# Kernel optimization log

Hardware: AMD Instinct MI355X
Metric: run time of the kernel (lower is better)

Reference implementation:

```python
import jax, jax.numpy as jnp
import numpy as np

B, N, D = 16, 8192, 256
H = D // 2
N_PARCELS = 64          # number of parcel labels in the stage lookup
K_PER_PARCEL = 32       # allocation m for every parcel (self.values)
TAU = 1.0               # gumbel-softmax temperature


def setup_inputs() -> dict:
    key = jax.random.key(0)
    ks = jax.random.split(key, 6)
    patches = jax.random.normal(ks[0], (B, N, D), dtype=jnp.float32)
    features = jax.random.normal(ks[1], (B, N, D), dtype=jnp.float32)
    W1 = jax.random.normal(ks[2], (D, H), dtype=jnp.float32) * 0.05
    b1 = jnp.zeros((H,), dtype=jnp.float32)
    W2 = jax.random.normal(ks[3], (H,), dtype=jnp.float32) * 0.05  # fc2 weight, out_dim=1 squeezed
    b2 = jnp.zeros((), dtype=jnp.float32)
    # pre-sampled Gumbel(0,1) noise (torch F.gumbel_softmax samples internally)
    gumbel = jax.random.gumbel(ks[4], (B, N), dtype=jnp.float32)
    # flat per-patch parcel label, identical across batch (lookup.reshape(-1)[:N])
    lookup = (jnp.arange(N, dtype=jnp.int32) % N_PARCELS)
    return {"patches": patches, "features": features, "W1": W1, "b1": b1,
            "W2": W2, "b2": b2, "gumbel": gumbel, "lookup": lookup}


def reference(patches, features, W1, b1, W2, b2, gumbel, lookup):
    # tiny MLP: fc1 -> relu -> fc2 -> squeeze(-1)
    hidden = jax.nn.relu(jnp.einsum('bnd,dh->bnh', features, W1) + b1)
    importance_logits = jnp.einsum('bnh,h->bn', hidden, W2) + b2          # [B, N]
    # soft gumbel-softmax scores over the patch axis
    scores = jax.nn.softmax((importance_logits + gumbel) / TAU, axis=-1)  # [B, N]

    labels = jnp.arange(N_PARCELS, dtype=lookup.dtype)

    def per_parcel(label):
        m = lookup == label                                # [N], same for all batches
        masked = jnp.where(m[None, :], scores, -jnp.inf)   # [B, N]
        _, idx = jax.lax.top_k(masked, K_PER_PARCEL)       # [B, K]
        return idx

    idx_pbk = jax.vmap(per_parcel)(labels)                 # [P, B, K]
    all_selected_indices = jnp.transpose(idx_pbk, (1, 0, 2)).reshape(B, N_PARCELS * K_PER_PARCEL)

    # scatter 1.0 at selected positions
    final_mask = jnp.zeros_like(scores).at[jnp.arange(B)[:, None], all_selected_indices].set(1.0)
    # straight-through: value == final_mask, grad flows as -d(logits)
    mask_grad = final_mask + jax.lax.stop_gradient(importance_logits) - importance_logits

    final_patches = patches * mask_grad[..., None]                         # [B, N, D]
    selected_patches = jnp.take_along_axis(final_patches, all_selected_indices[..., None], axis=1)
    return selected_patches, all_selected_indices, importance_logits
```

## Files before the change

kernel.cpp:

```cpp
#include <hip/hip_runtime.h>
#include <hip/hip_bf16.h>

#define NB 16
#define NN 8192
#define ND 256
#define NH 128
#define NPARCEL 64
#define KSEL 32

typedef __attribute__((ext_vector_type(8))) short short8;
typedef __attribute__((ext_vector_type(4))) float floatx4;
typedef __attribute__((ext_vector_type(4))) float f32x4;

__device__ __forceinline__ unsigned short f2b(float x) {
    unsigned u = __builtin_bit_cast(unsigned, x);
    u += 0x7fffu + ((u >> 16) & 1u);
    return (unsigned short)(u >> 16);
}
__device__ __forceinline__ float b2f(unsigned short h) {
    return __builtin_bit_cast(float, (unsigned)h << 16);
}


__global__ __launch_bounds__(256) void k_prep(const float* __restrict__ W1,
                                              unsigned short* __restrict__ W1Th,
                                              unsigned short* __restrict__ W1Tl) {
    int i = blockIdx.x * 256 + threadIdx.x;
    int k = i >> 7;
    int h = i & 127;
    float w = W1[i];
    unsigned short hi = f2b(w);
    float r = w - b2f(hi);
    W1Th[h * ND + k] = hi;
    W1Tl[h * ND + k] = f2b(r);
}

__global__ __launch_bounds__(256) void k_mlp(const float* __restrict__ feat,
                                             const unsigned short* __restrict__ W1Th,
                                             const unsigned short* __restrict__ W1Tl,
                                             const float* __restrict__ b1,
                                             const float* __restrict__ W2,
                                             const float* __restrict__ b2,
                                             const float* __restrict__ gum,
                                             float* __restrict__ z,
                                             float* __restrict__ out_logit) {
    const int wave = threadIdx.x >> 6;
    const int lane = threadIdx.x & 63;
    const int quad = lane >> 4;
    const int m    = lane & 15;
    const int wavebase = blockIdx.x * 128 + wave * 32;

    const unsigned short* bhb = W1Th + m * ND + quad * 8;
    const unsigned short* blb = W1Tl + m * ND + quad * 8;
    const float* ap0 = feat + (size_t)(wavebase + m) * ND + quad * 8;
    const float* ap1 = ap0 + 16 * ND;

    floatx4 acc[2][8];
#pragma unroll
    for (int rg = 0; rg < 2; ++rg)
#pragma unroll
        for (int nt = 0; nt < 8; ++nt) acc[rg][nt] = (floatx4){0.f, 0.f, 0.f, 0.f};

#pragma unroll
    for (int k0 = 0; k0 < ND; k0 += 32) {
        short8 bh[8], bl[8];
#pragma unroll
        for (int nt = 0; nt < 8; ++nt) {
            bh[nt] = *(const short8*)(bhb + nt * 16 * ND + k0);
            bl[nt] = *(const short8*)(blb + nt * 16 * ND + k0);
        }
#pragma unroll
        for (int rg = 0; rg < 2; ++rg) {
            const float* ap = (rg ? ap1 : ap0) + k0;
            f32x4 av0 = *(const f32x4*)(ap);
            f32x4 av1 = *(const f32x4*)(ap + 4);
            short8 ah, al;
#pragma unroll
            for (int j = 0; j < 8; ++j) {
                float x = (j < 4) ? av0[j] : av1[j - 4];
                unsigned short hb = f2b(x);
                ah[j] = (short)hb;
                al[j] = (short)f2b(x - b2f(hb));
            }
#pragma unroll
            for (int nt = 0; nt < 8; ++nt)
                acc[rg][nt] = __builtin_amdgcn_mfma_f32_16x16x32_bf16(ah, bh[nt], acc[rg][nt], 0, 0, 0);
#pragma unroll
            for (int nt = 0; nt < 8; ++nt)
                acc[rg][nt] = __builtin_amdgcn_mfma_f32_16x16x32_bf16(ah, bl[nt], acc[rg][nt], 0, 0, 0);
#pragma unroll
            for (int nt = 0; nt < 8; ++nt)
                acc[rg][nt] = __builtin_amdgcn_mfma_f32_16x16x32_bf16(al, bh[nt], acc[rg][nt], 0, 0, 0);
        }
    }

    const float b2v = b2[0];
#pragma unroll
    for (int rg = 0; rg < 2; ++rg) {
        float s[4] = {0.f, 0.f, 0.f, 0.f};
#pragma unroll
        for (int nt = 0; nt < 8; ++nt) {
            float b1f = b1[nt * 16 + m];
            float w2f = W2[nt * 16 + m];
#pragma unroll
            for (int r = 0; r < 4; ++r) {
                float h = acc[rg][nt][r] + b1f;
                s[r] += (h > 0.f ? h : 0.f) * w2f;
            }
        }
#pragma unroll
        for (int off = 1; off < 16; off <<= 1) {
#pragma unroll
            for (int r = 0; r < 4; ++r) s[r] += __shfl_xor(s[r], off, 64);
        }
        if (m == 0) {
            int rowbase = wavebase + rg * 16 + quad * 4;
#pragma unroll
            for (int r = 0; r < 4; ++r) {
                int row = rowbase + r;
                float logit = s[r] + b2v;
                out_logit[row] = logit;
                z[row] = logit + gum[row];
            }
        }
    }
}

__global__ __launch_bounds__(64) void k_topk(const float* __restrict__ z,
                                             int* __restrict__ sel,
                                             float* __restrict__ out_idx) {
    const int b = blockIdx.x >> 6;
    const int p = blockIdx.x & 63;
    const int l = threadIdx.x;
    const float* zb = z + b * NN;
    int i0 = p + 64 * l;
    int i1 = i0 + 4096;
    float v0 = zb[i0];
    float v1 = zb[i1];
    const int obase = b * (NPARCEL * KSEL) + p * KSEL;

    for (int r = 0; r < KSEL; ++r) {
        float bv; int bi;
        if (v0 > v1 || (v0 == v1 && i0 < i1)) { bv = v0; bi = i0; }
        else                                  { bv = v1; bi = i1; }
#pragma unroll
        for (int off = 1; off < 64; off <<= 1) {
            float ov = __shfl_xor(bv, off, 64);
            int   oi = __shfl_xor(bi, off, 64);
            if (ov > bv || (ov == bv && oi < bi)) { bv = ov; bi = oi; }
        }
        if      (bi == i0) { v0 = -__builtin_inff(); i0 = 0x7fffffff; }
        else if (bi == i1) { v1 = -__builtin_inff(); i1 = 0x7fffffff; }
        if (l == r) {
            int safe = bi & (NN - 1);
            sel[obase + r] = safe;
            out_idx[obase + r] = (float)safe;
        }
    }
}

__global__ __launch_bounds__(256) void k_gather1(const float* __restrict__ patches,
                                                 const int* __restrict__ sel,
                                                 float* __restrict__ out) {
    const int t = threadIdx.x;
    const int g = t >> 6;
    const int l = t & 63;
    const int rowk = blockIdx.x * 4 + g;
    if (rowk >= 512 && rowk < 640) return;
    const int b = rowk >> 11;
    const int idx = sel[rowk] & (NN - 1);
    f32x4 v = *((const f32x4*)(patches + ((size_t)b * NN + idx) * ND) + l);
    *((f32x4*)(out + (size_t)rowk * ND) + l) = v;
}

__global__ __launch_bounds__(256) void k_gather2(const float* __restrict__ patches,
                                                 const int* __restrict__ sel,
                                                 float* __restrict__ out) {
    __shared__ int sel_s[128];
    const int t = threadIdx.x;
    if (t < 128) sel_s[t] = sel[512 + t] & (NN - 1);
    __syncthreads();
    const int g = t >> 6;
    const int l = t & 63;
#pragma unroll 4
    for (int it = 0; it < 32; ++it) {
        const int r = it * 4 + g;
        const int rowk = 512 + r;
        const int idx = sel_s[r];
        f32x4 v = *((const f32x4*)(patches + (size_t)idx * ND) + l);
        *((f32x4*)(out + (size_t)rowk * ND) + l) = v;
    }
}

extern "C" void kernel_launch(void* const* d_in, const int* in_sizes, int n_in,
                              void* d_out, int out_size, void* d_ws, size_t ws_size,
                              hipStream_t stream) {
    const float* patches = (const float*)d_in[0];
    const float* feat    = (const float*)d_in[1];
    const float* W1      = (const float*)d_in[2];
    const float* b1      = (const float*)d_in[3];
    const float* W2      = (const float*)d_in[4];
    const float* b2      = (const float*)d_in[5];
    const float* gum     = (const float*)d_in[6];

    float* out       = (float*)d_out;
    float* out_sel   = out;
    float* out_idx   = out + 8388608;
    float* out_logit = out + 8388608 + 32768;

    float*          z    = out_sel;
    int*            sel  = (int*)(out_sel + 131072);
    unsigned short* W1Th = (unsigned short*)(out_sel + 163840);
    unsigned short* W1Tl = (unsigned short*)(out_sel + 180224);

    k_prep<<<128, 256, 0, stream>>>(W1, W1Th, W1Tl);
    k_mlp<<<(NB * NN) / 128, 256, 0, stream>>>(feat, W1Th, W1Tl, b1, W2, b2, gum, z, out_logit);
    k_topk<<<NB * NPARCEL, 64, 0, stream>>>(z, sel, out_idx);
    k_gather1<<<(NB * NPARCEL * KSEL) / 4, 256, 0, stream>>>(patches, sel, out_sel);
    k_gather2<<<1, 256, 0, stream>>>(patches, sel, out_sel);
}
```

Measured before the change: 357.1 us.

## Halve MLP grid with two-tile loop and stream W1 fragments per tile

The MLP kernel now launches half as many blocks, and each block loops over two 128-row tiles. Inside the K loop, the W1 hi/lo fragments are loaded per n-tile just before the MFMAs instead of being preloaded as 16 short8 registers. Both row groups are interleaved so each B fragment feeds six MFMAs. This cuts register pressure, which may raise occupancy, but it trades that for more scattered global/L2 loads of W1 and fewer blocks in flight.

```diff
diff --git a/kernel.cpp b/kernel.cpp
--- a/kernel.cpp
+++ b/kernel.cpp
@@ -48,79 +48,81 @@
     const int lane = threadIdx.x & 63;
     const int quad = lane >> 4;
     const int m    = lane & 15;
-    const int wavebase = blockIdx.x * 128 + wave * 32;
 
     const unsigned short* bhb = W1Th + m * ND + quad * 8;
     const unsigned short* blb = W1Tl + m * ND + quad * 8;
-    const float* ap0 = feat + (size_t)(wavebase + m) * ND + quad * 8;
-    const float* ap1 = ap0 + 16 * ND;
-
-    floatx4 acc[2][8];
-#pragma unroll
-    for (int rg = 0; rg < 2; ++rg)
-#pragma unroll
-        for (int nt = 0; nt < 8; ++nt) acc[rg][nt] = (floatx4){0.f, 0.f, 0.f, 0.f};
-
-#pragma unroll
-    for (int k0 = 0; k0 < ND; k0 += 32) {
-        short8 bh[8], bl[8];
-#pragma unroll
-        for (int nt = 0; nt < 8; ++nt) {
-            bh[nt] = *(const short8*)(bhb + nt * 16 * ND + k0);
-            bl[nt] = *(const short8*)(blb + nt * 16 * ND + k0);
-        }
+    const float b2v = b2[0];
+
+#pragma unroll 1
+    for (int t = 0; t < 2; ++t) {
+        const int wavebase = (blockIdx.x + t * 512) * 128 + wave * 32;
+        const float* ap0 = feat + (size_t)(wavebase + m) * ND + quad * 8;
+        const float* ap1 = ap0 + 16 * ND;
+
+        floatx4 acc[2][8];
+#pragma unroll
+        for (int rg = 0; rg < 2; ++rg)
+#pragma unroll
+            for (int nt = 0; nt < 8; ++nt) acc[rg][nt] = (floatx4){0.f, 0.f, 0.f, 0.f};
+
+#pragma unroll
+        for (int k0 = 0; k0 < ND; k0 += 32) {
+            f32x4 a00 = *(const f32x4*)(ap0 + k0);
+            f32x4 a01 = *(const f32x4*)(ap0 + k0 + 4);
+            f32x4 a10 = *(const f32x4*)(ap1 + k0);
+            f32x4 a11 = *(const f32x4*)(ap1 + k0 + 4);
+            short8 ah0, al0, ah1, al1;
+#pragma unroll
+            for (int j = 0; j < 8; ++j) {
+                float x0 = (j < 4) ? a00[j] : a01[j - 4];
+                unsigned short h0 = f2b(x0);
+                ah0[j] = (short)h0;
+                al0[j] = (short)f2b(x0 - b2f(h0));
+                float x1 = (j < 4) ? a10[j] : a11[j - 4];
+                unsigned short h1 = f2b(x1);
+                ah1[j] = (short)h1;
+                al1[j] = (short)f2b(x1 - b2f(h1));
+            }
+#pragma unroll
+            for (int nt = 0; nt < 8; ++nt) {
+                short8 bh = *(const short8*)(bhb + nt * 16 * ND + k0);
+                short8 bl = *(const short8*)(blb + nt * 16 * ND + k0);
+                acc[0][nt] = __builtin_amdgcn_mfma_f32_16x16x32_bf16(ah0, bh, acc[0][nt], 0, 0, 0);
+                acc[0][nt] = __builtin_amdgcn_mfma_f32_16x16x32_bf16(ah0, bl, acc[0][nt], 0, 0, 0);
+                acc[0][nt] = __builtin_amdgcn_mfma_f32_16x16x32_bf16(al0, bh, acc[0][nt], 0, 0, 0);
+                acc[1][nt] = __builtin_amdgcn_mfma_f32_16x16x32_bf16(ah1, bh, acc[1][nt], 0, 0, 0);
+                acc[1][nt] = __builtin_amdgcn_mfma_f32_16x16x32_bf16(ah1, bl, acc[1][nt], 0, 0, 0);
+                acc[1][nt] = __builtin_amdgcn_mfma_f32_16x16x32_bf16(al1, bh, acc[1][nt], 0, 0, 0);
+            }
+        }
+
 #pragma unroll
         for (int rg = 0; rg < 2; ++rg) {
-            const float* ap = (rg ? ap1 : ap0) + k0;
-            f32x4 av0 = *(const f32x4*)(ap);
-            f32x4 av1 = *(const f32x4*)(ap + 4);
-            short8 ah, al;
-#pragma unroll
-            for (int j = 0; j < 8; ++j) {
-                float x = (j < 4) ? av0[j] : av1[j - 4];
-                unsigned short hb = f2b(x);
-                ah[j] = (short)hb;
-                al[j] = (short)f2b(x - b2f(hb));
-            }
-#pragma unroll
-            for (int nt = 0; nt < 8; ++nt)
-                acc[rg][nt] = __builtin_amdgcn_mfma_f32_16x16x32_bf16(ah, bh[nt], acc[rg][nt], 0, 0, 0);
-#pragma unroll
-            for (int nt = 0; nt < 8; ++nt)
-                acc[rg][nt] = __builtin_amdgcn_mfma_f32_16x16x32_bf16(ah, bl[nt], acc[rg][nt], 0, 0, 0);
-#pragma unroll
-            for (int nt = 0; nt < 8; ++nt)
-                acc[rg][nt] = __builtin_amdgcn_mfma_f32_16x16x32_bf16(al, bh[nt], acc[rg][nt], 0, 0, 0);
-        }
-    }
-
-    const float b2v = b2[0];
-#pragma unroll
-    for (int rg = 0; rg < 2; ++rg) {
-        float s[4] = {0.f, 0.f, 0.f, 0.f};
-#pragma unroll
-        for (int nt = 0; nt < 8; ++nt) {
-            float b1f = b1[nt * 16 + m];
-            float w2f = W2[nt * 16 + m];
-#pragma unroll
-            for (int r = 0; r < 4; ++r) {
-                float h = acc[rg][nt][r] + b1f;
-                s[r] += (h > 0.f ? h : 0.f) * w2f;
-            }
-        }
-#pragma unroll
-        for (int off = 1; off < 16; off <<= 1) {
-#pragma unroll
-            for (int r = 0; r < 4; ++r) s[r] += __shfl_xor(s[r], off, 64);
-        }
-        if (m == 0) {
-            int rowbase = wavebase + rg * 16 + quad * 4;
-#pragma unroll
-            for (int r = 0; r < 4; ++r) {
-                int row = rowbase + r;
-                float logit = s[r] + b2v;
-                out_logit[row] = logit;
-                z[row] = logit + gum[row];
+            float s[4] = {0.f, 0.f, 0.f, 0.f};
+#pragma unroll
+            for (int nt = 0; nt < 8; ++nt) {
+                float b1f = b1[nt * 16 + m];
+                float w2f = W2[nt * 16 + m];
+#pragma unroll
+                for (int r = 0; r < 4; ++r) {
+                    float h = acc[rg][nt][r] + b1f;
+                    s[r] += (h > 0.f ? h : 0.f) * w2f;
+                }
+            }
+#pragma unroll
+            for (int off = 1; off < 16; off <<= 1) {
+#pragma unroll
+                for (int r = 0; r < 4; ++r) s[r] += __shfl_xor(s[r], off, 64);
+            }
+            if (m == 0) {
+                int rowbase = wavebase + rg * 16 + quad * 4;
+#pragma unroll
+                for (int r = 0; r < 4; ++r) {
+                    int row = rowbase + r;
+                    float logit = s[r] + b2v;
+                    out_logit[row] = logit;
+                    z[row] = logit + gum[row];
+                }
             }
         }
     }
@@ -214,7 +216,7 @@
     unsigned short* W1Tl = (unsigned short*)(out_sel + 180224);
 
     k_prep<<<128, 256, 0, stream>>>(W1, W1Th, W1Tl);
-    k_mlp<<<(NB * NN) / 128, 256, 0, stream>>>(feat, W1Th, W1Tl, b1, W2, b2, gum, z, out_logit);
+    k_mlp<<<(NB * NN) / 128 / 2, 256, 0, stream>>>(feat, W1Th, W1Tl, b1, W2, b2, gum, z, out_logit);
     k_topk<<<NB * NPARCEL, 64, 0, stream>>>(z, sel, out_idx);
     k_gather1<<<(NB * NPARCEL * KSEL) / 4, 256, 0, stream>>>(patches, sel, out_sel);
     k_gather2<<<1, 256, 0, stream>>>(patches, sel, out_sel);
```

Measured after the change: 406.2 us. +13.7%, slower.
